# Performance work log

Hardware: AMD Instinct MI355X
Metric: run time of the kernel (lower is better)

Reference implementation:

```python
import math
import jax, jax.numpy as jnp
import numpy as np

NP_, NA_ = 100000, 50000
IN_DIM = OUT_DIM = 128
H, DK = 4, 32
E_CITES, E_WRITES, E_REV = 600000, 300000, 300000


def setup_inputs() -> dict:
    key = jax.random.key(0)
    ks = jax.random.split(key, 16)
    s_in = 1.0 / math.sqrt(IN_DIM)   # ~ Linear default init scale
    s_dk = 1.0 / math.sqrt(DK)       # ~ xavier for d_k x d_k
    return {
        "h_paper": jax.random.normal(ks[0], (NP_, IN_DIM), jnp.float32),
        "h_author": jax.random.normal(ks[1], (NA_, IN_DIM), jnp.float32),
        "Wk": jax.random.normal(ks[2], (2, OUT_DIM, IN_DIM), jnp.float32) * s_in,
        "bk": jnp.zeros((2, OUT_DIM), jnp.float32),
        "Wq": jax.random.normal(ks[3], (2, OUT_DIM, IN_DIM), jnp.float32) * s_in,
        "bq": jnp.zeros((2, OUT_DIM), jnp.float32),
        "Wv": jax.random.normal(ks[4], (2, OUT_DIM, IN_DIM), jnp.float32) * s_in,
        "bv": jnp.zeros((2, OUT_DIM), jnp.float32),
        "Wa": jax.random.normal(ks[5], (2, OUT_DIM, OUT_DIM), jnp.float32) * s_in,
        "ba": jnp.zeros((2, OUT_DIM), jnp.float32),
        "rel_att": jax.random.normal(ks[6], (3, H, DK, DK), jnp.float32) * s_dk,
        "rel_msg": jax.random.normal(ks[7], (3, H, DK, DK), jnp.float32) * s_dk,
        "rel_pri": jnp.ones((3, H), jnp.float32),
        "skip": jnp.ones((2,), jnp.float32),
        "cites_src": jax.random.randint(ks[8], (E_CITES,), 0, NP_, jnp.int32),
        "cites_dst": jax.random.randint(ks[9], (E_CITES,), 0, NP_, jnp.int32),
        "writes_src": jax.random.randint(ks[10], (E_WRITES,), 0, NA_, jnp.int32),
        "writes_dst": jax.random.randint(ks[11], (E_WRITES,), 0, NP_, jnp.int32),
        "rev_src": jax.random.randint(ks[12], (E_REV,), 0, NP_, jnp.int32),
        "rev_dst": jax.random.randint(ks[13], (E_REV,), 0, NA_, jnp.int32),
    }


def _seg_softmax(scores, seg, n):
    # edge softmax normalized by destination node (DGL edge_softmax, norm_by='dst')
    m = jax.ops.segment_max(scores, seg, num_segments=n)
    e = jnp.exp(scores - m[seg])
    z = jax.ops.segment_sum(e, seg, num_segments=n)
    return e / z[seg]


def reference(h_paper, h_author, Wk, bk, Wq, bq, Wv, bv, Wa, ba,
              rel_att, rel_msg, rel_pri, skip,
              cites_src, cites_dst, writes_src, writes_dst, rev_src, rev_dst):
    sqrt_dk = math.sqrt(DK)

    def proj(h, W, b, t):
        return (h @ W[t].T + b[t]).reshape(-1, H, DK)  # [N, H, dk]

    def rel_agg(h_src, h_dst, ts, td, e, src, dst, n_dst):
        # relation-specific transforms of k and v (per-head dk x dk matmul)
        k = jnp.einsum('nhi,hij->nhj', proj(h_src, Wk, bk, ts), rel_att[e])
        v = jnp.einsum('nhi,hij->nhj', proj(h_src, Wv, bv, ts), rel_msg[e])
        q = proj(h_dst, Wq, bq, td)
        # per-edge attention logits: (q_dst . k_src) * pri / sqrt(dk)  -> [E, H]
        score = jnp.einsum('ehd,ehd->eh', q[dst], k[src]) * rel_pri[e] / sqrt_dk
        a = _seg_softmax(score, dst, n_dst)
        # weighted scatter-sum of messages to destination nodes
        return jax.ops.segment_sum(v[src] * a[:, :, None], dst, num_segments=n_dst)

    # cross_reducer='mean': average per-relation aggregates per dst node type
    t_paper = (rel_agg(h_paper, h_paper, 0, 0, 0, cites_src, cites_dst, NP_) +
               rel_agg(h_author, h_paper, 1, 0, 1, writes_src, writes_dst, NP_)) * 0.5
    t_author = rel_agg(h_paper, h_author, 0, 1, 2, rev_src, rev_dst, NA_)

    def out(t, h, nt):
        trans = t.reshape(-1, OUT_DIM) @ Wa[nt].T + ba[nt]  # dropout = identity (eval)
        alpha = jax.nn.sigmoid(skip[nt])
        return trans * alpha + h * (1.0 - alpha)

    return jnp.concatenate([out(t_paper, h_paper, 0), out(t_author, h_author, 1)], axis=0)
```

## Files before the change

### kernel.cpp

```cpp
#include <hip/hip_runtime.h>
#include <hip/hip_bf16.h>
#include <math.h>

#define NP 100000
#define NA 50000
#define DIM 128
#define NH 4
#define DKK 32
#define EC 600000
#define EW 300000
#define ER 300000
#define CAP 32
#define SCL 0.17677669529663687f

#define CDIV(a,b) (((a)+(b)-1)/(b))

typedef __attribute__((ext_vector_type(8))) short bf16x8;
typedef __attribute__((ext_vector_type(4))) float f32x4;
typedef __attribute__((ext_vector_type(2))) float f32x2;

__device__ __forceinline__ ushort f2b(float f){
  unsigned u = __float_as_uint(f);
  unsigned r = u + 0x7FFFu + ((u>>16)&1u);
  return (ushort)(r>>16);
}
__device__ __forceinline__ float blo(unsigned u){ return __uint_as_float(u<<16); }
__device__ __forceinline__ float bhi(unsigned u){ return __uint_as_float(u & 0xFFFF0000u); }

struct C2Args { const float4* in[2]; uint2* out[2]; };
__global__ void k_cast2(C2Args a){
  int s = blockIdx.y;
  int i = blockIdx.x*256 + threadIdx.x;
  float4 v = a.in[s][i];
  uint2 o;
  o.x = (unsigned)f2b(v.x) | ((unsigned)f2b(v.y)<<16);
  o.y = (unsigned)f2b(v.z) | ((unsigned)f2b(v.w)<<16);
  a.out[s][i] = o;
}

__global__ void k_zero_i(int* p, int n){
  int i = blockIdx.x*blockDim.x + threadIdx.x;
  if (i < n) p[i] = 0;
}

__global__ void k_fuse(const float* __restrict__ Wk, const float* __restrict__ bk,
                       const float* __restrict__ Wv, const float* __restrict__ bv,
                       const float* __restrict__ rel_att, const float* __restrict__ rel_msg,
                       ushort* __restrict__ Wfb_all, float* __restrict__ bfu_all){
  int rel = blockIdx.x >> 7;
  int ts = (rel==1) ? 1 : 0;
  ushort* Wfb = Wfb_all + rel*32768;
  float*  bfu = bfu_all + rel*256;
  int idx = (blockIdx.x & 127)*256 + threadIdx.x;
  int which = idx >> 14;
  int rem = idx & 16383;
  int op = rem >> 7;
  int j  = rem & 127;
  int h = op >> 5, jp = op & 31;
  const float* W  = which ? Wv : Wk;
  const float* R  = which ? rel_msg : rel_att;
  const float* Wt = W + (size_t)ts*DIM*DIM;
  const float* Re = R + (((size_t)rel*NH + h)*DKK)*DKK + jp;
  float acc = 0.f;
  #pragma unroll
  for (int i=0;i<DKK;i++) acc += Wt[(h*DKK+i)*DIM + j] * Re[(size_t)i*DKK];
  Wfb[which*16384 + op*DIM + j] = f2b(acc);
  if (idx < 256){
    int w2 = idx >> 7; int op2 = idx & 127; int h2 = op2>>5, jp2 = op2&31;
    const float* bsrc = (w2 ? bv : bk) + (size_t)ts*DIM;
    const float* R2 = (w2 ? rel_msg : rel_att) + (((size_t)rel*NH + h2)*DKK)*DKK + jp2;
    float accb = 0.f;
    #pragma unroll
    for (int i=0;i<DKK;i++) accb += bsrc[h2*DKK+i]*R2[(size_t)i*DKK];
    bfu[w2*DIM + op2] = accb;
  }
}

struct MArgs {
  const float* X[3];
  const ushort* W[3][3];
  const float* b[3][3];
  ushort* Y[3][3];
  int ystride[3][3];
  int N[3];
  int npan[3];
  int base[3];
};
__global__ __launch_bounds__(512) void k_mega(MArgs g){
  int b = blockIdx.x;
  int seg = (b >= g.base[2]) ? 2 : ((b >= g.base[1]) ? 1 : 0);
  int local = b - g.base[seg];
  int N = g.N[seg];
  int tile = local*64;
  if (tile >= N) return;
  int tid = threadIdx.x;
  int wv = tid >> 6, l = tid & 63;
  int lr = l & 15, lk = l >> 4;
  int rowg = wv >> 1, colg = wv & 1;
  int arow = tile + rowg*16 + lr;
  int ar = (arow < N) ? arow : 0;
  const float4* Ar = (const float4*)(g.X[seg] + (size_t)ar*DIM);
  bf16x8 A[4];
  #pragma unroll
  for (int kc=0;kc<4;kc++){
    float4 u = Ar[kc*8 + lk*2];
    float4 v = Ar[kc*8 + lk*2 + 1];
    bf16x8 a;
    a[0]=(short)f2b(u.x); a[1]=(short)f2b(u.y); a[2]=(short)f2b(u.z); a[3]=(short)f2b(u.w);
    a[4]=(short)f2b(v.x); a[5]=(short)f2b(v.y); a[6]=(short)f2b(v.z); a[7]=(short)f2b(v.w);
    A[kc] = a;
  }
  __shared__ __align__(16) ushort Wl[128*136];
  __shared__ __align__(16) ushort Ost[64*136];
  uint4* Wl4 = (uint4*)Wl;
  int npan = g.npan[seg];
  for (int p=0; p<npan; ++p){
    const uint4* Ws = (const uint4*)g.W[seg][p];
    #pragma unroll
    for (int i=0;i<4;i++){
      int idx = i*512 + tid;
      uint4 v = Ws[idx];
      int r = idx >> 4, c = idx & 15;
      Wl4[r*17 + c] = v;
    }
    __syncthreads();
    const float* bias = g.b[seg][p];
    #pragma unroll
    for (int ct=0; ct<4; ct++){
      int col = colg*64 + ct*16 + lr;
      f32x4 acc = {0.f,0.f,0.f,0.f};
      #pragma unroll
      for (int kc=0;kc<4;kc++){
        bf16x8 B = *(const bf16x8*)&Wl[col*136 + kc*32 + lk*8];
        acc = __builtin_amdgcn_mfma_f32_16x16x32_bf16(A[kc], B, acc, 0, 0, 0);
      }
      float bv = bias[col];
      #pragma unroll
      for (int j=0;j<4;j++)
        Ost[(rowg*16 + lk*4 + j)*136 + col] = f2b(acc[j] + bv);
    }
    __syncthreads();
    int orow = tid >> 3;
    int oseg = (tid & 7)*2;
    int grow = tile + orow;
    if (grow < N){
      uint4* dst = (uint4*)(g.Y[seg][p] + (size_t)grow*g.ystride[seg][p]);
      const uint4* s = (const uint4*)Ost;
      dst[oseg]   = s[orow*17 + oseg];
      dst[oseg+1] = s[orow*17 + oseg + 1];
    }
    __syncthreads();
  }
}

struct BArgs { const int* dst[3]; const int* src[3]; int* cnt[3]; int* slots[3]; int E[3]; int n[3]; };
__global__ void k_bucket(BArgs a){
  int r = blockIdx.y;
  int E = a.E[r], n = a.n[r];
  const int* dst = a.dst[r];
  const int* srcv = a.src[r];
  int* cnt = a.cnt[r];
  int* slots = a.slots[r];
  int g = blockIdx.x & 7;
  int sub = blockIdx.x >> 3;
  int chunk = (n + 7) >> 3;
  int lo = g*chunk;
  int hi = lo + chunk; if (hi > n) hi = n;
  int per = (E + 255) >> 8;
  per = (per + 3) & ~3;
  int e0 = sub*per;
  int e1 = e0 + per; if (e1 > E) e1 = E;
  for (int i = e0 + threadIdx.x*4; i < e1; i += 256*4){
    if (i + 4 <= e1){
      int4 d = *(const int4*)(dst + i);
      int4 s = *(const int4*)(srcv + i);
      if (d.x>=lo && d.x<hi){ int p=atomicAdd(&cnt[d.x],1); if(p<CAP) slots[(size_t)d.x*CAP+p]=s.x; }
      if (d.y>=lo && d.y<hi){ int p=atomicAdd(&cnt[d.y],1); if(p<CAP) slots[(size_t)d.y*CAP+p]=s.y; }
      if (d.z>=lo && d.z<hi){ int p=atomicAdd(&cnt[d.z],1); if(p<CAP) slots[(size_t)d.z*CAP+p]=s.z; }
      if (d.w>=lo && d.w<hi){ int p=atomicAdd(&cnt[d.w],1); if(p<CAP) slots[(size_t)d.w*CAP+p]=s.w; }
    } else {
      for (int j=i; j<e1; ++j){
        int d = dst[j];
        if (d>=lo && d<hi){ int p=atomicAdd(&cnt[d],1); if(p<CAP) slots[(size_t)d*CAP+p]=srcv[j]; }
      }
    }
  }
}

__device__ __forceinline__ void agg_step4(const unsigned* __restrict__ KV,
    const int4* __restrict__ sl4,
    int i, int deg, int nsrc, float qx, float qy, int lane,
    f32x2& av, float& z)
{
  int4 s4 = sl4[i>>2];
  int s0 = ((unsigned)s4.x < (unsigned)nsrc) ? s4.x : 0;
  int s1 = ((unsigned)s4.y < (unsigned)nsrc) ? s4.y : 0;
  int s2 = ((unsigned)s4.z < (unsigned)nsrc) ? s4.z : 0;
  int s3 = ((unsigned)s4.w < (unsigned)nsrc) ? s4.w : 0;
  bool v1 = (i+1 < deg), v2 = (i+2 < deg), v3 = (i+3 < deg);
  const unsigned* r0 = KV + (size_t)s0*128;
  const unsigned* r1 = KV + (size_t)s1*128;
  const unsigned* r2 = KV + (size_t)s2*128;
  const unsigned* r3 = KV + (size_t)s3*128;
  unsigned ku0 = r0[lane];
  unsigned ku1 = r1[lane];
  unsigned ku2 = r2[lane];
  unsigned ku3 = r3[lane];
  unsigned vu0 = r0[64 + lane];
  unsigned vu1 = r1[64 + lane];
  unsigned vu2 = r2[64 + lane];
  unsigned vu3 = r3[64 + lane];
  float p0 = qx*blo(ku0) + qy*bhi(ku0);
  float p1 = qx*blo(ku1) + qy*bhi(ku1);
  float p2 = qx*blo(ku2) + qy*bhi(ku2);
  float p3 = qx*blo(ku3) + qy*bhi(ku3);
  #pragma unroll
  for (int d=1; d<16; d<<=1){
    p0 += __shfl_xor(p0, d);
    p1 += __shfl_xor(p1, d);
    p2 += __shfl_xor(p2, d);
    p3 += __shfl_xor(p3, d);
  }
  float e0 = __expf(p0);
  float e1 = v1 ? __expf(p1) : 0.f;
  float e2 = v2 ? __expf(p2) : 0.f;
  float e3 = v3 ? __expf(p3) : 0.f;
  z += (e0+e1)+(e2+e3);
  f32x2 w0 = {blo(vu0), bhi(vu0)};
  f32x2 w1 = {blo(vu1), bhi(vu1)};
  f32x2 w2 = {blo(vu2), bhi(vu2)};
  f32x2 w3 = {blo(vu3), bhi(vu3)};
  av += (w0*e0 + w1*e1) + (w2*e2 + w3*e3);
}

__global__ __launch_bounds__(256) void k_attnM2(
    const unsigned* __restrict__ QP, const unsigned* __restrict__ QA,
    const unsigned* __restrict__ KV0, const unsigned* __restrict__ KV1,
    const unsigned* __restrict__ KV2,
    const int* __restrict__ slots_all, const int* __restrict__ cnt_all,
    const float* __restrict__ pri, float* __restrict__ t_paper, float* __restrict__ t_author)
{
  int w = blockIdx.x*4 + (threadIdx.x>>6);
  if (w >= NP+NA) return;
  int lane = threadIdx.x & 63;
  int h = lane >> 4;
  if (w < NP){
    unsigned qu = QP[(size_t)w*64 + lane];
    float qx = blo(qu), qy = bhi(qu);
    float s0f = pri[h]*SCL, s1f = pri[NH+h]*SCL;
    float qx0 = qx*s0f, qy0 = qy*s0f;
    float qx1 = qx*s1f, qy1 = qy*s1f;
    int d0 = cnt_all[w];      if (d0 > CAP) d0 = CAP;
    int d1 = cnt_all[NP + w]; if (d1 > CAP) d1 = CAP;
    const int4* sl0 = (const int4*)(slots_all + (size_t)w*CAP);
    const int4* sl1 = (const int4*)(slots_all + ((size_t)NP+w)*CAP);
    f32x2 x = {0.f,0.f}, y = {0.f,0.f};
    float zx = 0.f, zy = 0.f;
    int nmax = (d0 > d1) ? d0 : d1;
    for (int i = 0; i < nmax; i += 4){
      if (i < d0) agg_step4(KV0, sl0, i, d0, NP, qx0, qy0, lane, x, zx);
      if (i < d1) agg_step4(KV1, sl1, i, d1, NA, qx1, qy1, lane, y, zy);
    }
    float ix = (zx > 0.f) ? 1.f/zx : 0.f;
    float iy = (zy > 0.f) ? 1.f/zy : 0.f;
    f32x2 o = x*ix + y*iy;
    ((f32x2*)t_paper)[(size_t)w*64 + lane] = o;
  } else {
    int wn = w - NP;
    unsigned qu = QA[(size_t)wn*64 + lane];
    float qx = blo(qu), qy = bhi(qu);
    float s2f = pri[2*NH+h]*SCL;
    float qx2 = qx*s2f, qy2 = qy*s2f;
    int d2 = cnt_all[2*NP + wn]; if (d2 > CAP) d2 = CAP;
    const int4* sl2 = (const int4*)(slots_all + ((size_t)2*NP+wn)*CAP);
    f32x2 r = {0.f,0.f};
    float zr = 0.f;
    for (int i = 0; i < d2; i += 4)
      agg_step4(KV2, sl2, i, d2, NP, qx2, qy2, lane, r, zr);
    float ir = (zr > 0.f) ? 1.f/zr : 0.f;
    f32x2 o = r*ir;
    ((f32x2*)t_author)[(size_t)wn*64 + lane] = o;
  }
}

struct FArgs { const float* X[2]; const ushort* W[2]; const float* b[2]; const float* h[2];
               float* out[2]; float scale[2]; int N[2]; const float* skip; };
__global__ __launch_bounds__(256) void k_fingemm(FArgs g){
  int y = blockIdx.y;
  int N = g.N[y];
  if ((int)blockIdx.x*32 >= N) return;
  const float* X = g.X[y];
  const ushort* Wb = g.W[y];
  const float* bias = g.b[y];
  const float* hin = g.h[y];
  float* out = g.out[y];
  float scale = g.scale[y];
  int tid = threadIdx.x;
  int wv = tid >> 6;
  int l  = tid & 63;
  int lr = l & 15, lk = l >> 4;
  int r0 = blockIdx.x*32 + (wv&1)*16;
  int c0 = (wv>>1)*64;
  int arow = r0 + lr;
  int ar = (arow < N) ? arow : 0;
  const float4* Ar = (const float4*)(X + (size_t)ar*DIM);
  bf16x8 A[4];
  #pragma unroll
  for (int kc=0;kc<4;kc++){
    float4 u = Ar[kc*8 + lk*2];
    float4 v = Ar[kc*8 + lk*2 + 1];
    bf16x8 a;
    a[0]=(short)f2b(u.x); a[1]=(short)f2b(u.y); a[2]=(short)f2b(u.z); a[3]=(short)f2b(u.w);
    a[4]=(short)f2b(v.x); a[5]=(short)f2b(v.y); a[6]=(short)f2b(v.z); a[7]=(short)f2b(v.w);
    A[kc] = a;
  }
  __shared__ float Ls[32][132];
  #pragma unroll
  for (int ct=0; ct<4; ct++){
    int col = c0 + ct*16 + lr;
    const bf16x8* Wrow = (const bf16x8*)(Wb + (size_t)col*DIM);
    f32x4 acc = {0.f,0.f,0.f,0.f};
    #pragma unroll
    for (int kc=0;kc<4;kc++)
      acc = __builtin_amdgcn_mfma_f32_16x16x32_bf16(A[kc], Wrow[kc*4+lk], acc, 0, 0, 0);
    float bv = bias[col];
    #pragma unroll
    for (int j=0;j<4;j++){
      int lrow = (wv&1)*16 + lk*4 + j;
      Ls[lrow][col] = scale*acc[j] + bv;
    }
  }
  __syncthreads();
  float alpha = 1.f/(1.f + expf(-g.skip[y]));
  float beta  = 1.f - alpha;
  int orow = tid >> 3;
  int ocb  = (tid & 7)*16;
  int row  = blockIdx.x*32 + orow;
  if (row < N){
    const float4* H4 = (const float4*)hin;
    float4* O4 = (float4*)out;
    #pragma unroll
    for (int q=0;q<4;q++){
      float4 tv = *(const float4*)&Ls[orow][ocb + q*4];
      float4 hv = H4[(size_t)row*32 + (ocb>>2) + q];
      float4 o;
      o.x = alpha*tv.x + beta*hv.x;
      o.y = alpha*tv.y + beta*hv.y;
      o.z = alpha*tv.z + beta*hv.z;
      o.w = alpha*tv.w + beta*hv.w;
      O4[(size_t)row*32 + (ocb>>2) + q] = o;
    }
  }
}

extern "C" void kernel_launch(void* const* d_in, const int* in_sizes, int n_in,
                              void* d_out, int out_size, void* d_ws, size_t ws_size,
                              hipStream_t stream) {
  const float* h_paper = (const float*)d_in[0];
  const float* h_author= (const float*)d_in[1];
  const float* Wk = (const float*)d_in[2];
  const float* bk = (const float*)d_in[3];
  const float* Wq = (const float*)d_in[4];
  const float* bq = (const float*)d_in[5];
  const float* Wv = (const float*)d_in[6];
  const float* bv = (const float*)d_in[7];
  const float* Wa = (const float*)d_in[8];
  const float* ba = (const float*)d_in[9];
  const float* rel_att = (const float*)d_in[10];
  const float* rel_msg = (const float*)d_in[11];
  const float* rel_pri = (const float*)d_in[12];
  const float* skip    = (const float*)d_in[13];
  const int* cites_src = (const int*)d_in[14];
  const int* cites_dst = (const int*)d_in[15];
  const int* writes_src= (const int*)d_in[16];
  const int* writes_dst= (const int*)d_in[17];
  const int* rev_src   = (const int*)d_in[18];
  const int* rev_dst   = (const int*)d_in[19];

  ushort* qbP = (ushort*)d_ws;
  ushort* qbA = qbP + (size_t)NP*DIM;
  ushort* KV0 = qbA + (size_t)NA*DIM;
  ushort* KV1 = KV0 + (size_t)NP*256;
  ushort* KV2 = KV1 + (size_t)NA*256;
  ushort* Wqb = KV2 + (size_t)NP*256;
  ushort* Wab = Wqb + 32768;
  ushort* Wfb = Wab + 32768;
  float*  bfu = (float*)(Wfb + 3*32768);
  int* ib = (int*)(bfu + 3*256);
  const int NDST_TOT = 2*NP + NA;
  int* cnt_all   = ib;           ib += NDST_TOT;
  int* slots_all = ib;

  float* t_paper  = (float*)d_out;
  float* t_author = (float*)d_out + (size_t)NP*DIM;

  const int cntB[3] = {0, NP, 2*NP};

  {
    C2Args a;
    a.in[0]=(const float4*)Wq; a.out[0]=(uint2*)Wqb;
    a.in[1]=(const float4*)Wa; a.out[1]=(uint2*)Wab;
    k_cast2<<<dim3(32,2),256,0,stream>>>(a);
  }
  k_fuse<<<384,256,0,stream>>>(Wk, bk, Wv, bv, rel_att, rel_msg, Wfb, bfu);
  k_zero_i<<<CDIV(NDST_TOT,256),256,0,stream>>>(cnt_all, NDST_TOT);
  {
    BArgs b;
    const int* dsts[3] = {cites_dst, writes_dst, rev_dst};
    const int* srcs[3] = {cites_src, writes_src, rev_src};
    int Es[3] = {EC, EW, ER};
    int ns[3] = {NP, NP, NA};
    for (int r=0;r<3;r++){
      b.dst[r]=dsts[r]; b.src[r]=srcs[r];
      b.cnt[r]=cnt_all+cntB[r];
      b.slots[r]=slots_all+(size_t)cntB[r]*CAP;
      b.E[r]=Es[r]; b.n[r]=ns[r];
    }
    k_bucket<<<dim3(2048,3),256,0,stream>>>(b);
  }
  {
    const int T0 = CDIV(NP,64), T1 = CDIV(NA,64), T2 = CDIV(NP,64);
    MArgs m;
    m.base[0]=0; m.base[1]=T0; m.base[2]=T0+T1;
    m.X[0]=h_paper;  m.N[0]=NP; m.npan[0]=3;
    m.W[0][0]=Wqb;        m.b[0][0]=bq;        m.Y[0][0]=qbP;      m.ystride[0][0]=128;
    m.W[0][1]=Wfb;        m.b[0][1]=bfu;       m.Y[0][1]=KV0;      m.ystride[0][1]=256;
    m.W[0][2]=Wfb+16384;  m.b[0][2]=bfu+DIM;   m.Y[0][2]=KV0+128;  m.ystride[0][2]=256;
    m.X[1]=h_author; m.N[1]=NA; m.npan[1]=3;
    m.W[1][0]=Wqb+16384;        m.b[1][0]=bq+DIM;        m.Y[1][0]=qbA;      m.ystride[1][0]=128;
    m.W[1][1]=Wfb+32768;        m.b[1][1]=bfu+256;       m.Y[1][1]=KV1;      m.ystride[1][1]=256;
    m.W[1][2]=Wfb+32768+16384;  m.b[1][2]=bfu+256+DIM;   m.Y[1][2]=KV1+128;  m.ystride[1][2]=256;
    m.X[2]=h_paper;  m.N[2]=NP; m.npan[2]=2;
    m.W[2][0]=Wfb+2*32768;        m.b[2][0]=bfu+512;       m.Y[2][0]=KV2;      m.ystride[2][0]=256;
    m.W[2][1]=Wfb+2*32768+16384;  m.b[2][1]=bfu+512+DIM;   m.Y[2][1]=KV2+128;  m.ystride[2][1]=256;
    m.W[2][2]=Wfb;                m.b[2][2]=bfu;           m.Y[2][2]=KV2;      m.ystride[2][2]=256;
    k_mega<<<T0+T1+T2,512,0,stream>>>(m);
  }
  k_attnM2<<<CDIV(NP+NA,4),256,0,stream>>>(
      (const unsigned*)qbP, (const unsigned*)qbA,
      (const unsigned*)KV0, (const unsigned*)KV1, (const unsigned*)KV2,
      slots_all, cnt_all, rel_pri, t_paper, t_author);
  {
    FArgs f;
    f.X[0]=t_paper;   f.W[0]=Wab;        f.b[0]=ba;     f.h[0]=h_paper;
    f.out[0]=t_paper;  f.scale[0]=0.5f; f.N[0]=NP;
    f.X[1]=t_author;  f.W[1]=Wab+16384;  f.b[1]=ba+DIM; f.h[1]=h_author;
    f.out[1]=t_author; f.scale[1]=1.0f; f.N[1]=NA;
    f.skip = skip;
    k_fingemm<<<dim3(CDIV(NP,32),2),256,0,stream>>>(f);
  }
}
```

Before: 353.3 us.

## Fuse attention aggregation with output projection GEMM via shared-memory staging

Merges the per-node attention aggregation kernel and the final Wa projection/skip-mix kernel into one kernel. Each block aggregates 32 destination rows (4 waves × 8 passes) into shared memory, then runs the MFMA projection directly from that staged tile. This removes the fp32 round trip of t_paper/t_author through global memory and one kernel launch. In exchange, each block serialises 8 aggregation passes per wave, and the GEMM phase must wait for the slowest row, which may hurt latency hiding and load balance for gather-heavy work.

```diff
diff --git a/kernel.cpp b/kernel.cpp
--- a/kernel.cpp
+++ b/kernel.cpp
@@ -233,88 +233,89 @@
   av += (w0*e0 + w1*e1) + (w2*e2 + w3*e3);
 }
 
-__global__ __launch_bounds__(256) void k_attnM2(
-    const unsigned* __restrict__ QP, const unsigned* __restrict__ QA,
-    const unsigned* __restrict__ KV0, const unsigned* __restrict__ KV1,
-    const unsigned* __restrict__ KV2,
-    const int* __restrict__ slots_all, const int* __restrict__ cnt_all,
-    const float* __restrict__ pri, float* __restrict__ t_paper, float* __restrict__ t_author)
-{
-  int w = blockIdx.x*4 + (threadIdx.x>>6);
-  if (w >= NP+NA) return;
-  int lane = threadIdx.x & 63;
+struct AFArgs {
+  const unsigned *QP, *QA, *KV0, *KV1, *KV2;
+  const int *slots, *cnt;
+  const float *pri;
+  const ushort *WaP, *WaA;
+  const float *baP, *baA;
+  const float *hP, *hA;
+  float *outP, *outA;
+  const float *skip;
+  int PB;
+};
+__global__ __launch_bounds__(256) void k_attnfin(AFArgs a){
+  bool isP = (blockIdx.x < (unsigned)a.PB);
+  int wbase = isP ? blockIdx.x*32 : (blockIdx.x - a.PB)*32;
+  int N = isP ? NP : NA;
+  int tid = threadIdx.x;
+  int wid = tid >> 6;
+  int lane = tid & 63;
   int h = lane >> 4;
-  if (w < NP){
-    unsigned qu = QP[(size_t)w*64 + lane];
-    float qx = blo(qu), qy = bhi(qu);
-    float s0f = pri[h]*SCL, s1f = pri[NH+h]*SCL;
-    float qx0 = qx*s0f, qy0 = qy*s0f;
-    float qx1 = qx*s1f, qy1 = qy*s1f;
-    int d0 = cnt_all[w];      if (d0 > CAP) d0 = CAP;
-    int d1 = cnt_all[NP + w]; if (d1 > CAP) d1 = CAP;
-    const int4* sl0 = (const int4*)(slots_all + (size_t)w*CAP);
-    const int4* sl1 = (const int4*)(slots_all + ((size_t)NP+w)*CAP);
-    f32x2 x = {0.f,0.f}, y = {0.f,0.f};
-    float zx = 0.f, zy = 0.f;
-    int nmax = (d0 > d1) ? d0 : d1;
-    for (int i = 0; i < nmax; i += 4){
-      if (i < d0) agg_step4(KV0, sl0, i, d0, NP, qx0, qy0, lane, x, zx);
-      if (i < d1) agg_step4(KV1, sl1, i, d1, NA, qx1, qy1, lane, y, zy);
-    }
-    float ix = (zx > 0.f) ? 1.f/zx : 0.f;
-    float iy = (zy > 0.f) ? 1.f/zy : 0.f;
-    f32x2 o = x*ix + y*iy;
-    ((f32x2*)t_paper)[(size_t)w*64 + lane] = o;
-  } else {
-    int wn = w - NP;
-    unsigned qu = QA[(size_t)wn*64 + lane];
-    float qx = blo(qu), qy = bhi(qu);
-    float s2f = pri[2*NH+h]*SCL;
-    float qx2 = qx*s2f, qy2 = qy*s2f;
-    int d2 = cnt_all[2*NP + wn]; if (d2 > CAP) d2 = CAP;
-    const int4* sl2 = (const int4*)(slots_all + ((size_t)2*NP+wn)*CAP);
-    f32x2 r = {0.f,0.f};
-    float zr = 0.f;
-    for (int i = 0; i < d2; i += 4)
-      agg_step4(KV2, sl2, i, d2, NP, qx2, qy2, lane, r, zr);
-    float ir = (zr > 0.f) ? 1.f/zr : 0.f;
-    f32x2 o = r*ir;
-    ((f32x2*)t_author)[(size_t)wn*64 + lane] = o;
-  }
-}
-
-struct FArgs { const float* X[2]; const ushort* W[2]; const float* b[2]; const float* h[2];
-               float* out[2]; float scale[2]; int N[2]; const float* skip; };
-__global__ __launch_bounds__(256) void k_fingemm(FArgs g){
-  int y = blockIdx.y;
-  int N = g.N[y];
-  if ((int)blockIdx.x*32 >= N) return;
-  const float* X = g.X[y];
-  const ushort* Wb = g.W[y];
-  const float* bias = g.b[y];
-  const float* hin = g.h[y];
-  float* out = g.out[y];
-  float scale = g.scale[y];
-  int tid = threadIdx.x;
-  int wv = tid >> 6;
-  int l  = tid & 63;
-  int lr = l & 15, lk = l >> 4;
-  int r0 = blockIdx.x*32 + (wv&1)*16;
-  int c0 = (wv>>1)*64;
-  int arow = r0 + lr;
-  int ar = (arow < N) ? arow : 0;
-  const float4* Ar = (const float4*)(X + (size_t)ar*DIM);
+  __shared__ float Ls[32][132];
+  for (int pass = 0; pass < 8; ++pass){
+    int row = pass*4 + wid;
+    int w = wbase + row;
+    if (w < N){
+      f32x2 o;
+      if (isP){
+        unsigned qu = a.QP[(size_t)w*64 + lane];
+        float qx = blo(qu), qy = bhi(qu);
+        float s0f = a.pri[h]*SCL, s1f = a.pri[NH+h]*SCL;
+        float qx0 = qx*s0f, qy0 = qy*s0f;
+        float qx1 = qx*s1f, qy1 = qy*s1f;
+        int d0 = a.cnt[w];      if (d0 > CAP) d0 = CAP;
+        int d1 = a.cnt[NP + w]; if (d1 > CAP) d1 = CAP;
+        const int4* sl0 = (const int4*)(a.slots + (size_t)w*CAP);
+        const int4* sl1 = (const int4*)(a.slots + ((size_t)NP+w)*CAP);
+        f32x2 x = {0.f,0.f}, y = {0.f,0.f};
+        float zx = 0.f, zy = 0.f;
+        int nmax = (d0 > d1) ? d0 : d1;
+        for (int i = 0; i < nmax; i += 4){
+          if (i < d0) agg_step4(a.KV0, sl0, i, d0, NP, qx0, qy0, lane, x, zx);
+          if (i < d1) agg_step4(a.KV1, sl1, i, d1, NA, qx1, qy1, lane, y, zy);
+        }
+        float ix = (zx > 0.f) ? 1.f/zx : 0.f;
+        float iy = (zy > 0.f) ? 1.f/zy : 0.f;
+        o = x*ix + y*iy;
+      } else {
+        unsigned qu = a.QA[(size_t)w*64 + lane];
+        float qx = blo(qu), qy = bhi(qu);
+        float s2f = a.pri[2*NH+h]*SCL;
+        float qx2 = qx*s2f, qy2 = qy*s2f;
+        int d2 = a.cnt[2*NP + w]; if (d2 > CAP) d2 = CAP;
+        const int4* sl2 = (const int4*)(a.slots + ((size_t)2*NP+w)*CAP);
+        f32x2 r = {0.f,0.f};
+        float zr = 0.f;
+        for (int i = 0; i < d2; i += 4)
+          agg_step4(a.KV2, sl2, i, d2, NP, qx2, qy2, lane, r, zr);
+        float ir = (zr > 0.f) ? 1.f/zr : 0.f;
+        o = r*ir;
+      }
+      *(f32x2*)&Ls[row][2*lane] = o;
+    }
+  }
+  __syncthreads();
+  const ushort* Wb  = isP ? a.WaP : a.WaA;
+  const float* bias = isP ? a.baP : a.baA;
+  const float* hin  = isP ? a.hP  : a.hA;
+  float* out        = isP ? a.outP : a.outA;
+  float scale       = isP ? 0.5f : 1.0f;
+  float alpha = 1.f/(1.f + expf(-a.skip[isP ? 0 : 1]));
+  float beta  = 1.f - alpha;
+  int lr = lane & 15, lk = lane >> 4;
+  int r0loc = (wid&1)*16;
+  int c0 = (wid>>1)*64;
   bf16x8 A[4];
   #pragma unroll
   for (int kc=0;kc<4;kc++){
-    float4 u = Ar[kc*8 + lk*2];
-    float4 v = Ar[kc*8 + lk*2 + 1];
-    bf16x8 a;
-    a[0]=(short)f2b(u.x); a[1]=(short)f2b(u.y); a[2]=(short)f2b(u.z); a[3]=(short)f2b(u.w);
-    a[4]=(short)f2b(v.x); a[5]=(short)f2b(v.y); a[6]=(short)f2b(v.z); a[7]=(short)f2b(v.w);
-    A[kc] = a;
-  }
-  __shared__ float Ls[32][132];
+    const float* src = &Ls[r0loc + lr][kc*32 + lk*8];
+    bf16x8 aa;
+    #pragma unroll
+    for (int j=0;j<8;j++) aa[j] = (short)f2b(src[j]);
+    A[kc] = aa;
+  }
+  __syncthreads();
   #pragma unroll
   for (int ct=0; ct<4; ct++){
     int col = c0 + ct*16 + lr;
@@ -326,16 +327,14 @@
     float bv = bias[col];
     #pragma unroll
     for (int j=0;j<4;j++){
-      int lrow = (wv&1)*16 + lk*4 + j;
+      int lrow = r0loc + lk*4 + j;
       Ls[lrow][col] = scale*acc[j] + bv;
     }
   }
   __syncthreads();
-  float alpha = 1.f/(1.f + expf(-g.skip[y]));
-  float beta  = 1.f - alpha;
   int orow = tid >> 3;
   int ocb  = (tid & 7)*16;
-  int row  = blockIdx.x*32 + orow;
+  int row  = wbase + orow;
   if (row < N){
     const float4* H4 = (const float4*)hin;
     float4* O4 = (float4*)out;
@@ -436,17 +435,20 @@
     m.W[2][2]=Wfb;                m.b[2][2]=bfu;           m.Y[2][2]=KV2;      m.ystride[2][2]=256;
     k_mega<<<T0+T1+T2,512,0,stream>>>(m);
   }
-  k_attnM2<<<CDIV(NP+NA,4),256,0,stream>>>(
-      (const unsigned*)qbP, (const unsigned*)qbA,
-      (const unsigned*)KV0, (const unsigned*)KV1, (const unsigned*)KV2,
-      slots_all, cnt_all, rel_pri, t_paper, t_author);
   {
-    FArgs f;
-    f.X[0]=t_paper;   f.W[0]=Wab;        f.b[0]=ba;     f.h[0]=h_paper;
-    f.out[0]=t_paper;  f.scale[0]=0.5f; f.N[0]=NP;
-    f.X[1]=t_author;  f.W[1]=Wab+16384;  f.b[1]=ba+DIM; f.h[1]=h_author;
-    f.out[1]=t_author; f.scale[1]=1.0f; f.N[1]=NA;
-    f.skip = skip;
-    k_fingemm<<<dim3(CDIV(NP,32),2),256,0,stream>>>(f);
-  }
-}
+    const int PB = CDIV(NP,32);
+    const int AB = CDIV(NA,32);
+    AFArgs a;
+    a.QP = (const unsigned*)qbP;  a.QA = (const unsigned*)qbA;
+    a.KV0 = (const unsigned*)KV0; a.KV1 = (const unsigned*)KV1; a.KV2 = (const unsigned*)KV2;
+    a.slots = slots_all; a.cnt = cnt_all;
+    a.pri = rel_pri;
+    a.WaP = Wab; a.WaA = Wab + 16384;
+    a.baP = ba;  a.baA = ba + DIM;
+    a.hP = h_paper; a.hA = h_author;
+    a.outP = t_paper; a.outA = t_author;
+    a.skip = skip;
+    a.PB = PB;
+    k_attnfin<<<PB+AB,256,0,stream>>>(a);
+  }
+}
```

After: 336.2 us. 4.8% less time.
